# Performance work log

Measured on AMD Instinct MI355X. Metric: run time of the kernel, lower is better.

The kernel has to match this reference:

```python
import jax, jax.numpy as jnp
import numpy as np

B, N, D, H, W, OUT = 2, 2048, 128, 8, 4, 256

def setup_inputs() -> dict:
    key = jax.random.key(0)
    ks = jax.random.split(key, 8)
    s = 0.02
    return {
        "nodefeatures": jax.random.normal(ks[0], (B, N, D), jnp.float32),
        "nodeadj": jax.random.uniform(ks[1], (B, N, N, W), jnp.float32),
        "Wq": jax.random.normal(ks[2], (H, D, D), jnp.float32) * s,
        "bq": jnp.zeros((H, D), jnp.float32),
        "Wk": jax.random.normal(ks[3], (H, D, D), jnp.float32) * s,
        "bk": jnp.zeros((H, D), jnp.float32),
        "Wv": jax.random.normal(ks[4], (H, D, D), jnp.float32) * s,
        "bv": jnp.zeros((H, D), jnp.float32),
        "Wout": jax.random.normal(ks[5], (H * D, OUT), jnp.float32) * s,
        "bout": jnp.zeros((OUT,), jnp.float32),
    }

def reference(nodefeatures, nodeadj, Wq, bq, Wk, bk, Wv, bv, Wout, bout):
    # Per-head linear projections, all heads at once: [B,H,N,D]
    q = jnp.einsum('bnd,hde->bhne', nodefeatures, Wq) + bq[None, :, None, :]
    k = jnp.einsum('bnd,hde->bhne', nodefeatures, Wk) + bk[None, :, None, :]
    v = jnp.einsum('bnd,hde->bhne', nodefeatures, Wv) + bv[None, :, None, :]
    # Original scales by k.shape[1]**0.5 == sqrt(N) (node count, not head dim)
    scores = jnp.einsum('bhnd,bhmd->bhnm', q, k) / jnp.sqrt(jnp.asarray(N, q.dtype))
    # (scores[...,None] * nodeadj).sum(-1) == scores * nodeadj.sum(-1)
    scores = scores * nodeadj.sum(-1)[:, None, :, :]  # [B,H,N,N]
    attn = jax.nn.softmax(scores, axis=-1)  # torch softmax(dim=2) on [B,N,N] == key axis
    o = jnp.einsum('bhnm,bhmd->bhnd', attn, v)
    o = jnp.moveaxis(o, 1, 2).reshape(B, N, H * D)  # concat heads along feature dim
    return o @ Wout + bout
```

## Files before the change

kernel.cpp:

```cpp
#include <hip/hip_runtime.h>
#include <hip/hip_bf16.h>

#define BB 2
#define NN 2048
#define DD 128
#define HH 8
#define OUTD 256
#define SCALE 0.022097086912079612f

typedef __bf16 bf16x8 __attribute__((ext_vector_type(8)));
typedef float f32x4 __attribute__((ext_vector_type(4)));
typedef _Float16 f16x4 __attribute__((ext_vector_type(4)));

__device__ __forceinline__ unsigned short f2bf(float f) {
    union { float f; unsigned int u; } v; v.f = f;
    unsigned int r = (v.u + 0x7FFFu + ((v.u >> 16) & 1u)) >> 16;
    return (unsigned short)r;
}
__device__ __forceinline__ float bf2f(unsigned short s) {
    union { unsigned int u; float f; } v; v.u = ((unsigned int)s) << 16;
    return v.f;
}
__device__ __forceinline__ void gl_lds16(const unsigned short* g, unsigned short* l) {
    __builtin_amdgcn_global_load_lds(
        (const __attribute__((address_space(1))) unsigned int*)g,
        (__attribute__((address_space(3))) unsigned int*)l,
        16, 0, 0);
}

__global__ void prep_kernel(const float* __restrict__ X,
                            const float* __restrict__ Wq,
                            const float* __restrict__ Wk,
                            const float* __restrict__ Wv,
                            const float* __restrict__ Wout,
                            unsigned short* __restrict__ Xb,
                            unsigned short* __restrict__ WT,
                            unsigned short* __restrict__ WoutT)
{
    const int NX  = BB * NN * DD;
    const int NW  = 3 * HH * DD * DD;
    const int NWO = (HH * DD) * OUTD;
    int idx = blockIdx.x * blockDim.x + threadIdx.x;
    if (idx < NX) {
        Xb[idx] = f2bf(X[idx]);
    } else if (idx < NX + NW) {
        int i = idx - NX;
        int mat = i / (HH * DD * DD);
        int r   = i % (HH * DD * DD);
        int h = r / (DD * DD);
        int j = r % (DD * DD);
        int e = j / DD;
        int d = j % DD;
        const float* Wm = (mat == 0) ? Wq : ((mat == 1) ? Wk : Wv);
        WT[i] = f2bf(Wm[h * DD * DD + d * DD + e]);
    } else if (idx < NX + NW + NWO) {
        int i = idx - NX - NW;
        int o = i / (HH * DD);
        int k = i % (HH * DD);
        WoutT[i] = f2bf(Wout[k * OUTD + o]);
    }
}

__global__ void adjsum_kernel(const float4* __restrict__ adj, unsigned short* __restrict__ s) {
    int idx = blockIdx.x * blockDim.x + threadIdx.x;
    float4 a = adj[idx];
    s[idx] = f2bf((a.x + a.y) + (a.z + a.w));
}

__global__ __launch_bounds__(256) void proj_kernel(
    const unsigned short* __restrict__ Xb,
    const unsigned short* __restrict__ WT,
    const float* __restrict__ bq, const float* __restrict__ bk, const float* __restrict__ bv,
    unsigned short* __restrict__ Qo, unsigned short* __restrict__ Ko,
    unsigned short* __restrict__ Vt)
{
    const int mat = blockIdx.z;
    const int bh  = blockIdx.y;
    const int b = bh >> 3, h = bh & 7;
    const int n0 = blockIdx.x * 64;
    const int tid = threadIdx.x;
    const int lane = tid & 63, wv = tid >> 6;
    const int m = lane & 15, quad = lane >> 4;

    __shared__ unsigned short Wlds[128 * 136];

    const unsigned short* Wg = WT + ((size_t)mat * HH + h) * (DD * DD);
    #pragma unroll
    for (int i = tid; i < 128 * 16; i += 256) {
        int r = i >> 4, c = i & 15;
        *(uint4*)&Wlds[r * 136 + c * 8] = *(const uint4*)(Wg + r * 128 + c * 8);
    }

    const int row = n0 + wv * 16 + m;
    const unsigned short* Xr = Xb + ((size_t)b * NN + row) * DD;
    bf16x8 af[4];
    #pragma unroll
    for (int kc = 0; kc < 4; ++kc)
        af[kc] = *(const bf16x8*)(Xr + kc * 32 + quad * 8);

    __syncthreads();

    f32x4 acc[8];
    #pragma unroll
    for (int et = 0; et < 8; ++et) acc[et] = (f32x4){0.f, 0.f, 0.f, 0.f};

    #pragma unroll
    for (int kc = 0; kc < 4; ++kc) {
        #pragma unroll
        for (int et = 0; et < 8; ++et) {
            bf16x8 bfrg = *(const bf16x8*)&Wlds[(et * 16 + m) * 136 + kc * 32 + quad * 8];
            acc[et] = __builtin_amdgcn_mfma_f32_16x16x32_bf16(af[kc], bfrg, acc[et], 0, 0, 0);
        }
    }

    const float* bias = (mat == 0) ? bq : ((mat == 1) ? bk : bv);
    if (mat != 2) {
        #pragma unroll
        for (int et = 0; et < 8; ++et) {
            int e = et * 16 + m;
            float bb = bias[h * DD + e];
            #pragma unroll
            for (int reg = 0; reg < 4; ++reg) {
                int r = n0 + wv * 16 + quad * 4 + reg;
                unsigned short v16 = f2bf(acc[et][reg] + bb);
                if (mat == 0) Qo[((size_t)bh * NN + r) * DD + e] = v16;
                else          Ko[((size_t)bh * NN + r) * DD + e] = v16;
            }
        }
    } else {
        __syncthreads();
        #pragma unroll
        for (int et = 0; et < 8; ++et) {
            int e = et * 16 + m;
            float bb = bias[h * DD + e];
            #pragma unroll
            for (int reg = 0; reg < 4; ++reg)
                Wlds[(wv * 16 + quad * 4 + reg) * 136 + e] = f2bf(acc[et][reg] + bb);
        }
        __syncthreads();
        const int e = tid >> 1, nh = tid & 1;
        #pragma unroll
        for (int j = 0; j < 4; ++j) {
            unsigned short tmp[8];
            #pragma unroll
            for (int kk = 0; kk < 8; ++kk)
                tmp[kk] = Wlds[(nh * 32 + j * 8 + kk) * 136 + e];
            *(uint4*)(Vt + ((size_t)bh * DD + e) * NN + n0 + nh * 32 + j * 8) = *(uint4*)tmp;
        }
    }
}

__global__ __launch_bounds__(256, 4) void attn_kernel(
    const unsigned short* __restrict__ Q,
    const unsigned short* __restrict__ K,
    const unsigned short* __restrict__ Vt,
    const unsigned short* __restrict__ adjs,
    _Float16* __restrict__ Opart,
    float* __restrict__ Lpart)
{
    const int x = blockIdx.x;
    const int h = blockIdx.y;
    const int ks = x & 1, qt = (x >> 1) & 31, b = x >> 6;
    const int bh = b * HH + h;
    const int q0 = qt * 64;
    const int kstart = ks * 1024;
    const int tid = threadIdx.x;
    const int lane = tid & 63, wv = tid >> 6;
    const int m = lane & 15, quad = lane >> 4;

    __shared__ unsigned short Kb[2][32 * 128];
    __shared__ unsigned short Vb[2][128 * 32];
    __shared__ unsigned short Plds[4][16 * 40];

    const unsigned short* Kbase = K + (size_t)bh * NN * DD;
    const unsigned short* Vbase = Vt + (size_t)bh * DD * NN;

    const int qrow = q0 + wv * 16 + m;
    const unsigned short* Qr = Q + ((size_t)bh * NN + qrow) * DD;
    bf16x8 qf[4];
    #pragma unroll
    for (int kc = 0; kc < 4; ++kc)
        qf[kc] = *(const bf16x8*)(Qr + kc * 32 + quad * 8);

    f32x4 o[8];
    #pragma unroll
    for (int dt = 0; dt < 8; ++dt) o[dt] = (f32x4){0.f, 0.f, 0.f, 0.f};
    float li[4] = {0.f, 0.f, 0.f, 0.f};

    const unsigned short* Abase = adjs + ((size_t)b * NN + q0 + wv * 16 + quad * 4) * NN;

    const int kr4 = lane >> 4, kc16 = lane & 15;
    const int vr16 = lane >> 2, vc4 = lane & 3;

    #define STAGE(buf, kbase_)                                                              \
        {                                                                                   \
            _Pragma("unroll")                                                               \
            for (int j2 = 0; j2 < 2; ++j2) {                                                \
                const int j = wv * 2 + j2;                                                  \
                const int krow = j * 4 + kr4;                                               \
                gl_lds16(Kbase + (size_t)((kbase_) + krow) * DD + ((kc16 ^ (krow & 15)) * 8),\
                         &Kb[buf][j * 512]);                                                \
                const int vrow = j * 16 + vr16;                                             \
                gl_lds16(Vbase + (size_t)vrow * NN + (kbase_) + ((vc4 ^ ((vr16 >> 1) & 3)) * 8),\
                         &Vb[buf][j * 512]);                                                \
            }                                                                               \
        }

    STAGE(0, kstart);
    __syncthreads();

    for (int kt = 0; kt < 32; ++kt) {
        const int cb = kt & 1, nb = cb ^ 1;
        const int k0 = kstart + kt * 32;

        float areg[2][4];
        #pragma unroll
        for (int nt = 0; nt < 2; ++nt)
            #pragma unroll
            for (int reg = 0; reg < 4; ++reg)
                areg[nt][reg] = bf2f(Abase[(size_t)reg * NN + k0 + nt * 16 + m]) * SCALE;

        if (kt + 1 < 32) STAGE(nb, k0 + 32);

        f32x4 s[2];
        s[0] = (f32x4){0.f, 0.f, 0.f, 0.f};
        s[1] = (f32x4){0.f, 0.f, 0.f, 0.f};
        #pragma unroll
        for (int kc = 0; kc < 4; ++kc) {
            #pragma unroll
            for (int nt = 0; nt < 2; ++nt) {
                bf16x8 kf = *(const bf16x8*)&Kb[cb][(nt * 16 + m) * 128 + (((kc * 4 + quad) ^ m) * 8)];
                s[nt] = __builtin_amdgcn_mfma_f32_16x16x32_bf16(qf[kc], kf, s[nt], 0, 0, 0);
            }
        }

        #pragma unroll
        for (int nt = 0; nt < 2; ++nt) {
            #pragma unroll
            for (int reg = 0; reg < 4; ++reg) {
                float p = __expf(s[nt][reg] * areg[nt][reg]);
                li[reg] += p;
                Plds[wv][(quad * 4 + reg) * 40 + nt * 16 + m] = f2bf(p);
            }
        }

        bf16x8 pf = *(const bf16x8*)&Plds[wv][m * 40 + quad * 8];
        #pragma unroll
        for (int dt = 0; dt < 8; ++dt) {
            bf16x8 vf = *(const bf16x8*)&Vb[cb][(dt * 16 + m) * 32 + ((quad ^ ((m >> 1) & 3)) * 8)];
            o[dt] = __builtin_amdgcn_mfma_f32_16x16x32_bf16(pf, vf, o[dt], 0, 0, 0);
        }

        __syncthreads();
    }
    #undef STAGE

    #pragma unroll
    for (int reg = 0; reg < 4; ++reg) {
        float t = li[reg];
        t += __shfl_xor(t, 1);
        t += __shfl_xor(t, 2);
        t += __shfl_xor(t, 4);
        t += __shfl_xor(t, 8);
        li[reg] = t;
    }
    const int rbase = q0 + wv * 16 + quad * 4;
    if (m == 0) {
        #pragma unroll
        for (int reg = 0; reg < 4; ++reg)
            Lpart[((size_t)ks * (BB * HH) + bh) * NN + rbase + reg] = li[reg];
    }
    #pragma unroll
    for (int reg = 0; reg < 4; ++reg) {
        const size_t obase = (((size_t)ks * (BB * HH) + bh) * NN + rbase + reg) * DD;
        #pragma unroll
        for (int dt = 0; dt < 8; ++dt)
            Opart[obase + dt * 16 + m] = (_Float16)o[dt][reg];
    }
}

__global__ void combine_kernel(const _Float16* __restrict__ Op,
                               const float* __restrict__ Lp,
                               unsigned short* __restrict__ Ocat)
{
    const int SPLIT_OFF = BB * HH * NN * DD;
    int t = blockIdx.x * blockDim.x + threadIdx.x;
    int e0 = t * 4;
    int row = e0 >> 7;
    float l = 1.0f / (Lp[row] + Lp[row + BB * HH * NN]);
    f16x4 a = *(const f16x4*)(Op + e0);
    f16x4 c = *(const f16x4*)(Op + SPLIT_OFF + e0);
    int bh = row >> 11, n = row & (NN - 1);
    int b = bh >> 3, h = bh & 7;
    size_t obase = ((size_t)(b * NN + n)) * (HH * DD) + h * DD + (e0 & (DD - 1));
    unsigned short u[4];
    #pragma unroll
    for (int i = 0; i < 4; ++i)
        u[i] = f2bf(((float)a[i] + (float)c[i]) * l);
    *(ushort4*)(Ocat + obase) = *(ushort4*)u;
}

__global__ __launch_bounds__(256) void out_kernel(
    const unsigned short* __restrict__ Ocat,
    const unsigned short* __restrict__ WoutT,
    const float* __restrict__ bout,
    float* __restrict__ out)
{
    const int m0 = blockIdx.x * 64;
    const int c0 = blockIdx.y * 64;
    const int tid = threadIdx.x;
    const int lane = tid & 63, wv = tid >> 6;
    const int m = lane & 15, quad = lane >> 4;

    __shared__ unsigned short Wlds[64 * 136];

    f32x4 acc[4];
    #pragma unroll
    for (int nt = 0; nt < 4; ++nt) acc[nt] = (f32x4){0.f, 0.f, 0.f, 0.f};

    const unsigned short* Orow = Ocat + (size_t)(m0 + wv * 16 + m) * (HH * DD);

    for (int kc = 0; kc < 8; ++kc) {
        #pragma unroll
        for (int i = tid; i < 64 * 16; i += 256) {
            int r = i >> 4, c = i & 15;
            *(uint4*)&Wlds[r * 136 + c * 8] =
                *(const uint4*)(WoutT + (size_t)(c0 + r) * (HH * DD) + kc * 128 + c * 8);
        }
        __syncthreads();
        #pragma unroll
        for (int j = 0; j < 4; ++j) {
            bf16x8 afr = *(const bf16x8*)(Orow + kc * 128 + j * 32 + quad * 8);
            #pragma unroll
            for (int nt = 0; nt < 4; ++nt) {
                bf16x8 bfr = *(const bf16x8*)&Wlds[(nt * 16 + m) * 136 + j * 32 + quad * 8];
                acc[nt] = __builtin_amdgcn_mfma_f32_16x16x32_bf16(afr, bfr, acc[nt], 0, 0, 0);
            }
        }
        __syncthreads();
    }

    #pragma unroll
    for (int nt = 0; nt < 4; ++nt) {
        int oc = c0 + nt * 16 + m;
        float bb = bout[oc];
        #pragma unroll
        for (int reg = 0; reg < 4; ++reg) {
            int r = m0 + wv * 16 + quad * 4 + reg;
            out[(size_t)r * OUTD + oc] = acc[nt][reg] + bb;
        }
    }
}

extern "C" void kernel_launch(void* const* d_in, const int* in_sizes, int n_in,
                              void* d_out, int out_size, void* d_ws, size_t ws_size,
                              hipStream_t stream)
{
    const float* X    = (const float*)d_in[0];
    const float* adj  = (const float*)d_in[1];
    const float* Wq   = (const float*)d_in[2];
    const float* bq   = (const float*)d_in[3];
    const float* Wk   = (const float*)d_in[4];
    const float* bk   = (const float*)d_in[5];
    const float* Wv   = (const float*)d_in[6];
    const float* bv   = (const float*)d_in[7];
    const float* Wout = (const float*)d_in[8];
    const float* bout = (const float*)d_in[9];
    float* out = (float*)d_out;

    char* ws = (char*)d_ws;
    unsigned short* Xb    = (unsigned short*)(ws);
    unsigned short* WT    = (unsigned short*)(ws + 1048576);
    unsigned short* WoutT = (unsigned short*)(ws + 1835008);
    unsigned short* Q     = (unsigned short*)(ws + 2359296);
    unsigned short* Kp    = (unsigned short*)(ws + 10747904);
    unsigned short* Vt    = (unsigned short*)(ws + 19136512);
    unsigned short* Ocat  = (unsigned short*)(ws + 27525120);
    unsigned short* AsumB = (unsigned short*)(ws + 35913728);
    _Float16*       Opart = (_Float16*)(ws + 52690944);
    float*          Lpart = (float*)(ws);

    prep_kernel<<<4608, 256, 0, stream>>>(X, Wq, Wk, Wv, Wout, Xb, WT, WoutT);
    adjsum_kernel<<<(BB * NN * NN) / 256, 256, 0, stream>>>((const float4*)adj, AsumB);
    proj_kernel<<<dim3(NN / 64, BB * HH, 3), 256, 0, stream>>>(Xb, WT, bq, bk, bv, Q, Kp, Vt);
    attn_kernel<<<dim3(128, HH), 256, 0, stream>>>(Q, Kp, Vt, AsumB, Opart, Lpart);
    combine_kernel<<<(BB * HH * NN * DD / 4) / 256, 256, 0, stream>>>(Opart, Lpart, Ocat);
    out_kernel<<<dim3((BB * NN) / 64, OUTD / 64), 256, 0, stream>>>(Ocat, WoutT, bout, out);
}
```

Baseline: 309.4 us.

## Process two 16-row query tiles per wave to reuse K/V tiles in attention

Each wave now handles 32 query rows instead of 16, so every attention block covers 128 queries and each K/V tile staged in LDS feeds twice as many MFMAs. This halves the grid to 512 blocks and halves the total K/V global traffic and LDS staging per query. In exchange, register pressure roughly doubles for the accumulators, launch bounds drop to 2 blocks per SM, and fewer blocks may leave some CUs underused on a 256-CU device.

```diff
diff --git a/kernel.cpp b/kernel.cpp
--- a/kernel.cpp
+++ b/kernel.cpp
@@ -150,7 +150,7 @@
     }
 }
 
-__global__ __launch_bounds__(256, 4) void attn_kernel(
+__global__ __launch_bounds__(256, 2) void attn_kernel(
     const unsigned short* __restrict__ Q,
     const unsigned short* __restrict__ K,
     const unsigned short* __restrict__ Vt,
@@ -160,9 +160,9 @@
 {
     const int x = blockIdx.x;
     const int h = blockIdx.y;
-    const int ks = x & 1, qt = (x >> 1) & 31, b = x >> 6;
+    const int ks = x & 1, qt = (x >> 1) & 15, b = x >> 5;
     const int bh = b * HH + h;
-    const int q0 = qt * 64;
+    const int q0 = qt * 128;
     const int kstart = ks * 1024;
     const int tid = threadIdx.x;
     const int lane = tid & 63, wv = tid >> 6;
@@ -170,24 +170,28 @@
 
     __shared__ unsigned short Kb[2][32 * 128];
     __shared__ unsigned short Vb[2][128 * 32];
-    __shared__ unsigned short Plds[4][16 * 40];
+    __shared__ unsigned short Plds[4][32 * 40];
 
     const unsigned short* Kbase = K + (size_t)bh * NN * DD;
     const unsigned short* Vbase = Vt + (size_t)bh * DD * NN;
 
-    const int qrow = q0 + wv * 16 + m;
-    const unsigned short* Qr = Q + ((size_t)bh * NN + qrow) * DD;
-    bf16x8 qf[4];
-    #pragma unroll
-    for (int kc = 0; kc < 4; ++kc)
-        qf[kc] = *(const bf16x8*)(Qr + kc * 32 + quad * 8);
-
-    f32x4 o[8];
-    #pragma unroll
-    for (int dt = 0; dt < 8; ++dt) o[dt] = (f32x4){0.f, 0.f, 0.f, 0.f};
-    float li[4] = {0.f, 0.f, 0.f, 0.f};
-
-    const unsigned short* Abase = adjs + ((size_t)b * NN + q0 + wv * 16 + quad * 4) * NN;
+    bf16x8 qf[2][4];
+    #pragma unroll
+    for (int nq = 0; nq < 2; ++nq) {
+        const unsigned short* Qr = Q + ((size_t)bh * NN + q0 + wv * 32 + nq * 16 + m) * DD;
+        #pragma unroll
+        for (int kc = 0; kc < 4; ++kc)
+            qf[nq][kc] = *(const bf16x8*)(Qr + kc * 32 + quad * 8);
+    }
+
+    f32x4 o[2][8];
+    #pragma unroll
+    for (int nq = 0; nq < 2; ++nq)
+        #pragma unroll
+        for (int dt = 0; dt < 8; ++dt) o[nq][dt] = (f32x4){0.f, 0.f, 0.f, 0.f};
+    float li[2][4] = {{0.f, 0.f, 0.f, 0.f}, {0.f, 0.f, 0.f, 0.f}};
+
+    const unsigned short* Abase = adjs + ((size_t)b * NN + q0 + wv * 32 + quad * 4) * NN;
 
     const int kr4 = lane >> 4, kc16 = lane & 15;
     const int vr16 = lane >> 2, vc4 = lane & 3;
@@ -213,42 +217,54 @@
         const int cb = kt & 1, nb = cb ^ 1;
         const int k0 = kstart + kt * 32;
 
-        float areg[2][4];
-        #pragma unroll
-        for (int nt = 0; nt < 2; ++nt)
-            #pragma unroll
-            for (int reg = 0; reg < 4; ++reg)
-                areg[nt][reg] = bf2f(Abase[(size_t)reg * NN + k0 + nt * 16 + m]) * SCALE;
+        float ar[2][2][4];
+        #pragma unroll
+        for (int nq = 0; nq < 2; ++nq)
+            #pragma unroll
+            for (int nt = 0; nt < 2; ++nt)
+                #pragma unroll
+                for (int reg = 0; reg < 4; ++reg)
+                    ar[nq][nt][reg] =
+                        bf2f(Abase[(size_t)(nq * 16 + reg) * NN + k0 + nt * 16 + m]) * SCALE;
 
         if (kt + 1 < 32) STAGE(nb, k0 + 32);
 
-        f32x4 s[2];
-        s[0] = (f32x4){0.f, 0.f, 0.f, 0.f};
-        s[1] = (f32x4){0.f, 0.f, 0.f, 0.f};
+        f32x4 s[2][2];
+        #pragma unroll
+        for (int nq = 0; nq < 2; ++nq)
+            #pragma unroll
+            for (int nt = 0; nt < 2; ++nt) s[nq][nt] = (f32x4){0.f, 0.f, 0.f, 0.f};
         #pragma unroll
         for (int kc = 0; kc < 4; ++kc) {
             #pragma unroll
             for (int nt = 0; nt < 2; ++nt) {
                 bf16x8 kf = *(const bf16x8*)&Kb[cb][(nt * 16 + m) * 128 + (((kc * 4 + quad) ^ m) * 8)];
-                s[nt] = __builtin_amdgcn_mfma_f32_16x16x32_bf16(qf[kc], kf, s[nt], 0, 0, 0);
+                s[0][nt] = __builtin_amdgcn_mfma_f32_16x16x32_bf16(qf[0][kc], kf, s[0][nt], 0, 0, 0);
+                s[1][nt] = __builtin_amdgcn_mfma_f32_16x16x32_bf16(qf[1][kc], kf, s[1][nt], 0, 0, 0);
             }
         }
 
         #pragma unroll
-        for (int nt = 0; nt < 2; ++nt) {
-            #pragma unroll
-            for (int reg = 0; reg < 4; ++reg) {
-                float p = __expf(s[nt][reg] * areg[nt][reg]);
-                li[reg] += p;
-                Plds[wv][(quad * 4 + reg) * 40 + nt * 16 + m] = f2bf(p);
+        for (int nq = 0; nq < 2; ++nq) {
+            #pragma unroll
+            for (int nt = 0; nt < 2; ++nt) {
+                #pragma unroll
+                for (int reg = 0; reg < 4; ++reg) {
+                    float p = __expf(s[nq][nt][reg] * ar[nq][nt][reg]);
+                    li[nq][reg] += p;
+                    Plds[wv][(nq * 16 + quad * 4 + reg) * 40 + nt * 16 + m] = f2bf(p);
+                }
             }
         }
 
-        bf16x8 pf = *(const bf16x8*)&Plds[wv][m * 40 + quad * 8];
+        bf16x8 pf[2];
+        pf[0] = *(const bf16x8*)&Plds[wv][(0 * 16 + m) * 40 + quad * 8];
+        pf[1] = *(const bf16x8*)&Plds[wv][(1 * 16 + m) * 40 + quad * 8];
         #pragma unroll
         for (int dt = 0; dt < 8; ++dt) {
             bf16x8 vf = *(const bf16x8*)&Vb[cb][(dt * 16 + m) * 32 + ((quad ^ ((m >> 1) & 3)) * 8)];
-            o[dt] = __builtin_amdgcn_mfma_f32_16x16x32_bf16(pf, vf, o[dt], 0, 0, 0);
+            o[0][dt] = __builtin_amdgcn_mfma_f32_16x16x32_bf16(pf[0], vf, o[0][dt], 0, 0, 0);
+            o[1][dt] = __builtin_amdgcn_mfma_f32_16x16x32_bf16(pf[1], vf, o[1][dt], 0, 0, 0);
         }
 
         __syncthreads();
@@ -256,26 +272,29 @@
     #undef STAGE
 
     #pragma unroll
-    for (int reg = 0; reg < 4; ++reg) {
-        float t = li[reg];
-        t += __shfl_xor(t, 1);
-        t += __shfl_xor(t, 2);
-        t += __shfl_xor(t, 4);
-        t += __shfl_xor(t, 8);
-        li[reg] = t;
-    }
-    const int rbase = q0 + wv * 16 + quad * 4;
-    if (m == 0) {
-        #pragma unroll
-        for (int reg = 0; reg < 4; ++reg)
-            Lpart[((size_t)ks * (BB * HH) + bh) * NN + rbase + reg] = li[reg];
-    }
-    #pragma unroll
-    for (int reg = 0; reg < 4; ++reg) {
-        const size_t obase = (((size_t)ks * (BB * HH) + bh) * NN + rbase + reg) * DD;
-        #pragma unroll
-        for (int dt = 0; dt < 8; ++dt)
-            Opart[obase + dt * 16 + m] = (_Float16)o[dt][reg];
+    for (int nq = 0; nq < 2; ++nq) {
+        #pragma unroll
+        for (int reg = 0; reg < 4; ++reg) {
+            float t = li[nq][reg];
+            t += __shfl_xor(t, 1);
+            t += __shfl_xor(t, 2);
+            t += __shfl_xor(t, 4);
+            t += __shfl_xor(t, 8);
+            li[nq][reg] = t;
+        }
+        const int rbase = q0 + wv * 32 + nq * 16 + quad * 4;
+        if (m == 0) {
+            #pragma unroll
+            for (int reg = 0; reg < 4; ++reg)
+                Lpart[((size_t)ks * (BB * HH) + bh) * NN + rbase + reg] = li[nq][reg];
+        }
+        #pragma unroll
+        for (int reg = 0; reg < 4; ++reg) {
+            const size_t obase = (((size_t)ks * (BB * HH) + bh) * NN + rbase + reg) * DD;
+            #pragma unroll
+            for (int dt = 0; dt < 8; ++dt)
+                Opart[obase + dt * 16 + m] = (_Float16)o[nq][dt][reg];
+        }
     }
 }
 
@@ -383,7 +402,7 @@
     prep_kernel<<<4608, 256, 0, stream>>>(X, Wq, Wk, Wv, Wout, Xb, WT, WoutT);
     adjsum_kernel<<<(BB * NN * NN) / 256, 256, 0, stream>>>((const float4*)adj, AsumB);
     proj_kernel<<<dim3(NN / 64, BB * HH, 3), 256, 0, stream>>>(Xb, WT, bq, bk, bv, Q, Kp, Vt);
-    attn_kernel<<<dim3(128, HH), 256, 0, stream>>>(Q, Kp, Vt, AsumB, Opart, Lpart);
+    attn_kernel<<<dim3(64, HH), 256, 0, stream>>>(Q, Kp, Vt, AsumB, Opart, Lpart);
     combine_kernel<<<(BB * HH * NN * DD / 4) / 256, 256, 0, stream>>>(Opart, Lpart, Ocat);
     out_kernel<<<dim3((BB * NN) / 64, OUTD / 64), 256, 0, stream>>>(Ocat, WoutT, bout, out);
 }
```

Measured after the change: 315.9 us. +2.1%, slower.

## Permute adjacency-sum layout so attention loads it with 16-byte vector reads

Applied to the files above, without the earlier changes.

The adjsum kernel now writes each 128-column group of summed adjacency values in a permuted order through shared memory, so every lane's scalars for several key tiles sit contiguously. The attention loop is split into groups of four key tiles, and each group loads four 16-byte vectors per lane instead of eight scattered 2-byte loads per tile. This cuts the number of small global loads in the inner loop. In exchange it adds an LDS round trip and a barrier to adjsum and keeps more registers live across four tiles.

```diff
diff --git a/kernel.cpp b/kernel.cpp
--- a/kernel.cpp
+++ b/kernel.cpp
@@ -11,6 +11,7 @@
 typedef __bf16 bf16x8 __attribute__((ext_vector_type(8)));
 typedef float f32x4 __attribute__((ext_vector_type(4)));
 typedef _Float16 f16x4 __attribute__((ext_vector_type(4)));
+typedef unsigned short u16x8 __attribute__((ext_vector_type(8)));
 
 __device__ __forceinline__ unsigned short f2bf(float f) {
     union { float f; unsigned int u; } v; v.f = f;
@@ -62,9 +63,16 @@
 }
 
 __global__ void adjsum_kernel(const float4* __restrict__ adj, unsigned short* __restrict__ s) {
-    int idx = blockIdx.x * blockDim.x + threadIdx.x;
+    __shared__ __align__(16) unsigned short ls[256];
+    const int tid = threadIdx.x;
+    const int idx = blockIdx.x * 256 + tid;
     float4 a = adj[idx];
-    s[idx] = f2bf((a.x + a.y) + (a.z + a.w));
+    const int k = tid & 127;
+    const int p = ((k & 15) << 3) + (((k >> 5) & 3) << 1) + ((k >> 4) & 1);
+    ls[(tid & 128) + p] = f2bf((a.x + a.y) + (a.z + a.w));
+    __syncthreads();
+    if (tid < 32)
+        *(uint4*)(s + (size_t)blockIdx.x * 256 + tid * 8) = *(const uint4*)&ls[tid * 8];
 }
 
 __global__ __launch_bounds__(256) void proj_kernel(
@@ -187,7 +195,8 @@
     for (int dt = 0; dt < 8; ++dt) o[dt] = (f32x4){0.f, 0.f, 0.f, 0.f};
     float li[4] = {0.f, 0.f, 0.f, 0.f};
 
-    const unsigned short* Abase = adjs + ((size_t)b * NN + q0 + wv * 16 + quad * 4) * NN;
+    const unsigned short* Ab =
+        adjs + ((size_t)(b * NN + q0 + wv * 16 + quad * 4)) * NN + kstart + m * 8;
 
     const int kr4 = lane >> 4, kc16 = lane & 15;
     const int vr16 = lane >> 2, vc4 = lane & 3;
@@ -209,49 +218,53 @@
     STAGE(0, kstart);
     __syncthreads();
 
-    for (int kt = 0; kt < 32; ++kt) {
-        const int cb = kt & 1, nb = cb ^ 1;
-        const int k0 = kstart + kt * 32;
-
-        float areg[2][4];
-        #pragma unroll
-        for (int nt = 0; nt < 2; ++nt)
-            #pragma unroll
-            for (int reg = 0; reg < 4; ++reg)
-                areg[nt][reg] = bf2f(Abase[(size_t)reg * NN + k0 + nt * 16 + m]) * SCALE;
-
-        if (kt + 1 < 32) STAGE(nb, k0 + 32);
-
-        f32x4 s[2];
-        s[0] = (f32x4){0.f, 0.f, 0.f, 0.f};
-        s[1] = (f32x4){0.f, 0.f, 0.f, 0.f};
-        #pragma unroll
-        for (int kc = 0; kc < 4; ++kc) {
+    u16x8 acur[4];
+
+    for (int g = 0; g < 8; ++g) {
+        #pragma unroll
+        for (int j = 0; j < 4; ++j)
+            acur[j] = *(const u16x8*)(Ab + (size_t)j * NN + g * 128);
+
+        #pragma unroll
+        for (int t = 0; t < 4; ++t) {
+            const int kt = g * 4 + t;
+            const int cb = kt & 1, nb = cb ^ 1;
+            const int k0 = kstart + kt * 32;
+
+            if (kt + 1 < 32) STAGE(nb, k0 + 32);
+
+            f32x4 s[2];
+            s[0] = (f32x4){0.f, 0.f, 0.f, 0.f};
+            s[1] = (f32x4){0.f, 0.f, 0.f, 0.f};
+            #pragma unroll
+            for (int kc = 0; kc < 4; ++kc) {
+                #pragma unroll
+                for (int nt = 0; nt < 2; ++nt) {
+                    bf16x8 kf = *(const bf16x8*)&Kb[cb][(nt * 16 + m) * 128 + (((kc * 4 + quad) ^ m) * 8)];
+                    s[nt] = __builtin_amdgcn_mfma_f32_16x16x32_bf16(qf[kc], kf, s[nt], 0, 0, 0);
+                }
+            }
+
             #pragma unroll
             for (int nt = 0; nt < 2; ++nt) {
-                bf16x8 kf = *(const bf16x8*)&Kb[cb][(nt * 16 + m) * 128 + (((kc * 4 + quad) ^ m) * 8)];
-                s[nt] = __builtin_amdgcn_mfma_f32_16x16x32_bf16(qf[kc], kf, s[nt], 0, 0, 0);
+                #pragma unroll
+                for (int reg = 0; reg < 4; ++reg) {
+                    float ar = bf2f(acur[reg][t * 2 + nt]) * SCALE;
+                    float p = __expf(s[nt][reg] * ar);
+                    li[reg] += p;
+                    Plds[wv][(quad * 4 + reg) * 40 + nt * 16 + m] = f2bf(p);
+                }
             }
-        }
-
-        #pragma unroll
-        for (int nt = 0; nt < 2; ++nt) {
-            #pragma unroll
-            for (int reg = 0; reg < 4; ++reg) {
-                float p = __expf(s[nt][reg] * areg[nt][reg]);
-                li[reg] += p;
-                Plds[wv][(quad * 4 + reg) * 40 + nt * 16 + m] = f2bf(p);
+
+            bf16x8 pf = *(const bf16x8*)&Plds[wv][m * 40 + quad * 8];
+            #pragma unroll
+            for (int dt = 0; dt < 8; ++dt) {
+                bf16x8 vf = *(const bf16x8*)&Vb[cb][(dt * 16 + m) * 32 + ((quad ^ ((m >> 1) & 3)) * 8)];
+                o[dt] = __builtin_amdgcn_mfma_f32_16x16x32_bf16(pf, vf, o[dt], 0, 0, 0);
             }
-        }
-
-        bf16x8 pf = *(const bf16x8*)&Plds[wv][m * 40 + quad * 8];
-        #pragma unroll
-        for (int dt = 0; dt < 8; ++dt) {
-            bf16x8 vf = *(const bf16x8*)&Vb[cb][(dt * 16 + m) * 32 + ((quad ^ ((m >> 1) & 3)) * 8)];
-            o[dt] = __builtin_amdgcn_mfma_f32_16x16x32_bf16(pf, vf, o[dt], 0, 0, 0);
-        }
-
-        __syncthreads();
+
+            __syncthreads();
+        }
     }
     #undef STAGE
 
```

New measurement: 328.6 us. 1.06x slower.
